# Optimization experiments

Measured on AMD Instinct MI355X. Metric: run time of the kernel, lower is better.

Reference implementation:

```python
import jax, jax.numpy as jnp
import numpy as np

B, T, D, H, C = 64, 512, 128, 512, 256  # batch, seq_len, input_dim, rnn_dim, clf hidden


def _lstm_cell(x, h, c, Wih, Whh, b):
    # PyTorch gate order: i, f, g, o; b = bias_ih + bias_hh
    gates = x @ Wih.T + h @ Whh.T + b  # [B, 4H]
    i, f, g, o = jnp.split(gates, 4, axis=-1)
    c = jax.nn.sigmoid(f) * c + jax.nn.sigmoid(i) * jnp.tanh(g)
    h = jax.nn.sigmoid(o) * jnp.tanh(c)
    return h, c


def _run_lstm2(xs, state, p0, p1):
    # xs: [B, T, in]; state: (h0, c0, h1, c1) each [B, H]
    def step(carry, x_t):
        h0, c0, h1, c1 = carry
        h0, c0 = _lstm_cell(x_t, h0, c0, *p0)
        h1, c1 = _lstm_cell(h0, h1, c1, *p1)
        return (h0, c0, h1, c1), h1
    state, ys = jax.lax.scan(step, state, jnp.swapaxes(xs, 0, 1))
    return jnp.swapaxes(ys, 0, 1), state


def setup_inputs() -> dict:
    key = jax.random.key(0)
    ks = jax.random.split(key, 18)
    s = 0.04  # ~1/sqrt(H), matches torch LSTM init scale
    w = lambda k, shape: (jax.random.normal(k, shape, jnp.float32) * s)
    inp = {
        "x": jax.random.uniform(ks[0], (B, T, D), dtype=jnp.float32),
        "y": (jax.random.uniform(ks[1], (B, T, D), dtype=jnp.float32) > 0.9).astype(jnp.float32),
        "enc_Wih0": w(ks[2], (4 * H, D)), "enc_Whh0": w(ks[3], (4 * H, H)), "enc_b0": w(ks[4], (4 * H,)),
        "enc_Wih1": w(ks[5], (4 * H, H)), "enc_Whh1": w(ks[6], (4 * H, H)), "enc_b1": w(ks[7], (4 * H,)),
        "dec_Wih0": w(ks[8], (4 * H, D)), "dec_Whh0": w(ks[9], (4 * H, H)), "dec_b0": w(ks[10], (4 * H,)),
        "dec_Wih1": w(ks[11], (4 * H, H)), "dec_Whh1": w(ks[12], (4 * H, H)), "dec_b1": w(ks[13], (4 * H,)),
        "clf_W1": w(ks[14], (C, H)), "clf_b1": w(ks[15], (C,)),
        "clf_W2": w(ks[16], (D, C)), "clf_b2": w(ks[17], (D,)),
    }
    return inp


def reference(x, y, enc_Wih0, enc_Whh0, enc_b0, enc_Wih1, enc_Whh1, enc_b1,
              dec_Wih0, dec_Whh0, dec_b0, dec_Wih1, dec_Whh1, dec_b1,
              clf_W1, clf_b1, clf_W2, clf_b2):
    Bc = x.shape[0]
    z = jnp.zeros((Bc, H), x.dtype)
    # encoder: only final (h, c) of both layers is used
    _, state = _run_lstm2(x, (z, z, z, z),
                          (enc_Wih0, enc_Whh0, enc_b0), (enc_Wih1, enc_Whh1, enc_b1))
    # decoder under full teacher forcing: steps t=1..T-1 consume y[:, t-1]
    dec_out, _ = _run_lstm2(y[:, :-1], state,
                            (dec_Wih0, dec_Whh0, dec_b0), (dec_Wih1, dec_Whh1, dec_b1))
    hid = jax.nn.relu(dec_out @ clf_W1.T + clf_b1)          # [B, T-1, C]
    logits = hid @ clf_W2.T + clf_b2                        # [B, T-1, D]
    # outputs[:, 0] stays zero, as in the torch loop starting at t=1
    return jnp.concatenate([jnp.zeros_like(logits[:, :1]), logits], axis=1)
```

## Files before the change

### kernel.cpp

```cpp
#include <hip/hip_runtime.h>
#include <hip/hip_bf16.h>
#include <stdint.h>

#define SMEM_BYTES 150528

using short8  = __attribute__((ext_vector_type(8))) short;
using f32x4   = __attribute__((ext_vector_type(4))) float;
using u32x4   = __attribute__((ext_vector_type(4))) unsigned int;

#define OXBF 0u
#define OYBF 8388608u
#define OWE0 16777216u
#define OWD0 (OWE0 + 2621440u)
#define OWE1 (OWD0 + 2621440u)
#define OWD1 (OWE1 + 4194304u)
#define OWC1 (OWD1 + 4194304u)
#define OWC2 (OWC1 + 262144u)
#define OH0  (OWC2 + 65536u)
#define OH1  (OH0 + 524288u)
#define OHP  (OH1 + 524288u)
#define OFLG (OHP + 262144u)
#define OFC1 (OFLG + 4096u)
#define OFH  (OFLG + 8192u)
#define OFL  (OFLG + 9216u)
#define OH1B (OFLG + 16384u)

static __device__ __forceinline__ unsigned short f2bf(float f){
  union { float f; unsigned u; } v; v.f = f;
  unsigned r = v.u + 0x7FFFu + ((v.u >> 16) & 1u);
  return (unsigned short)(r >> 16);
}
static __device__ __forceinline__ float sigm(float x){ return 1.f/(1.f+__expf(-x)); }
static __device__ __forceinline__ float tanh_(float x){ return 1.f - 2.f/(__expf(2.f*x)+1.f); }

static __device__ __forceinline__ u32x4 ld_cg16(const void* p){
  u32x4 v;
  asm volatile("global_load_dwordx4 %0, %1, off sc0 sc1" : "=v"(v) : "v"(p) : "memory");
  return v;
}
static __device__ __forceinline__ unsigned ld_cg4(const void* p){
  unsigned v;
  asm volatile("global_load_dword %0, %1, off sc0 sc1\n\ts_waitcnt vmcnt(0)"
               : "=v"(v) : "v"(p) : "memory");
  return v;
}
static __device__ __forceinline__ unsigned ld_cg4_async(const void* p){
  unsigned v;
  asm volatile("global_load_dword %0, %1, off sc0 sc1" : "=v"(v) : "v"(p) : "memory");
  return v;
}
static __device__ __forceinline__ void st_cg16(void* p, u32x4 v){
  asm volatile("global_store_dwordx4 %0, %1, off sc0 sc1" :: "v"(p), "v"(v) : "memory");
}
static __device__ __forceinline__ void st_cg4(void* p, unsigned v){
  asm volatile("global_store_dword %0, %1, off sc0 sc1" :: "v"(p), "v"(v) : "memory");
}
static __device__ __forceinline__ void drain_vm(){
  asm volatile("s_waitcnt vmcnt(0)" ::: "memory");
}
static __device__ __forceinline__ bool isS(u32x4 v){
  return (v[0]==0xFFFFFFFFu) | (v[1]==0xFFFFFFFFu) | (v[2]==0xFFFFFFFFu) | (v[3]==0xFFFFFFFFu);
}

__global__ void k_init(float* __restrict__ out, uint8_t* __restrict__ ws){
  int i = blockIdx.x*blockDim.x + threadIdx.x;
  int ns = gridDim.x*blockDim.x;
  uint32_t* r0 = (uint32_t*)(ws + OH0);
  uint32_t* r1 = (uint32_t*)(ws + OH1);
  const int slotw = 65536/4;
  for (int k=i; k<8*slotw; k+=ns){
    unsigned v = (k < 7*slotw) ? 0xFFFFFFFFu : 0u;
    r0[k] = v; r1[k] = v;
  }
  uint32_t* rb = (uint32_t*)(ws + OH1B);
  for (int k=i; k<8*slotw; k+=ns) rb[k] = 0xFFFFFFFFu;
  uint32_t* rp = (uint32_t*)(ws + OHP);
  for (int k=i; k<262144/4; k+=ns) rp[k] = 0xFFFFFFFFu;
  uint32_t* fl = (uint32_t*)(ws + OFLG);
  for (int k=i; k<16384/4; k+=ns) fl[k] = 0u;
  for (int k=i; k<64*128; k+=ns) out[(size_t)(k>>7)*(512*128) + (k&127)] = 0.f;
}

__global__ void k_cvt(const float* __restrict__ x, const float* __restrict__ y,
                      uint8_t* __restrict__ ws){
  unsigned short* xb = (unsigned short*)(ws + OXBF);
  unsigned short* yb = (unsigned short*)(ws + OYBF);
  const int n = 64*512*128;
  int i = blockIdx.x*blockDim.x + threadIdx.x, ns = gridDim.x*blockDim.x;
  for (int k=i; k<n; k+=ns){ xb[k] = f2bf(x[k]); yb[k] = f2bf(y[k]); }
}

__global__ void k_swzgate(const float* __restrict__ Wih, const float* __restrict__ Whh,
                          uint8_t* __restrict__ ws, size_t dstOff, int Kin, int KC, int NKK, int mode){
  unsigned short* dst = (unsigned short*)(ws + dstOff);
  const int total = 2048 * (KC*4);
  int i = blockIdx.x*blockDim.x + threadIdx.x, ns = gridDim.x*blockDim.x;
  for (int idx=i; idx<total; idx+=ns){
    int j = idx & 7;
    int lane = (idx >> 3) & 63;
    int t = idx >> 9;
    int g = t & 3; t >>= 2;
    int kk = t % NKK; t /= NKK;
    int w = t & 3; int ub = t >> 2;
    int off = ((lane>>4)<<3) + j;
    int k = mode ? (kk==0 ? w*32 + off : 128 + w*128 + (kk-1)*32 + off)
                 : (w*KC + kk*32 + off);
    int u = ub*16 + (lane&15);
    int row = g*512 + u;
    float v = (k < Kin) ? Wih[(size_t)row*Kin + k] : Whh[(size_t)row*512 + (k-Kin)];
    dst[idx] = f2bf(v);
  }
}

__global__ void k_swzclf(const float* __restrict__ W, uint8_t* __restrict__ ws,
                         size_t dstOff, int nwgs, int Kw, int Ktot){
  unsigned short* dst = (unsigned short*)(ws + dstOff);
  const int NKK = Kw/32;
  const int total = nwgs*4*NKK*64*8;
  int i = blockIdx.x*blockDim.x + threadIdx.x, ns = gridDim.x*blockDim.x;
  for (int idx=i; idx<total; idx+=ns){
    int j = idx & 7;
    int lane = (idx >> 3) & 63;
    int t = idx >> 9;
    int kk = t % NKK; t /= NKK;
    int w = t & 3; int wg = t >> 2;
    int k = w*Kw + kk*32 + ((lane>>4)<<3) + j;
    int col = wg*16 + (lane&15);
    dst[idx] = f2bf(W[(size_t)col*Ktot + k]);
  }
}

__launch_bounds__(256, 1)
__global__ void k_seq(uint8_t* __restrict__ ws,
                      const float* __restrict__ eb0, const float* __restrict__ eb1,
                      const float* __restrict__ db0, const float* __restrict__ db1,
                      const float* __restrict__ cb1, const float* __restrict__ cb2,
                      float* __restrict__ out){
  __shared__ uint8_t smem[SMEM_BYTES];
  const int wg = blockIdx.x, tid = threadIdx.x;
  const int w = tid>>6, l = tid&63, lr = l&15, lg = l>>4;

  const unsigned short* xb = (const unsigned short*)(ws+OXBF);
  const unsigned short* yb = (const unsigned short*)(ws+OYBF);
  unsigned short* h0r = (unsigned short*)(ws+OH0);
  unsigned short* h1r = (unsigned short*)(ws+OH1);
  unsigned short* h1b = (unsigned short*)(ws+OH1B);
  unsigned short* hpr = (unsigned short*)(ws+OHP);

  short8* BL = (short8*)smem;
  float*  P0 = (float*)(smem + 131072);
  float*  P1 = (float*)(smem + 139776);
  unsigned short* HS = (unsigned short*)(smem + 148480);

  const u32x4 S4 = (u32x4){0xFFFFFFFFu,0xFFFFFFFFu,0xFFFFFFFFu,0xFFFFFFFFu};

  auto loadB = [&](size_t srcOff, int bytes){
    const u32x4* s = (const u32x4*)(ws + srcOff);
    u32x4* d = (u32x4*)smem;
    for (int i = tid; i < bytes/16; i += 256) d[i] = s[i];
  };

  if (wg < 128){
    const bool isC0 = wg < 64;
    const int cwg = isC0 ? wg : wg-64;
    const int bt = cwg>>5, ub = cwg&31;
    const int u = tid&15, ug = ub*16 + u;
    const int bbytes = isC0 ? 81920 : 131072;

    float be[4], bd[4];
    {
      const float* e = isC0 ? eb0 : eb1;
      const float* d = isC0 ? db0 : db1;
      #pragma unroll
      for (int g=0; g<4; ++g){ be[g] = e[g*512+ug]; bd[g] = d[g*512+ug]; }
    }
    loadB((isC0 ? (size_t)OWE0 : (size_t)OWE1) + (size_t)ub*bbytes, bbytes);
    float cS0 = 0.f, cS1 = 0.f;
    __syncthreads();

    for (int t = 0; t < 1023; ++t){
      if (t == 512){
        __syncthreads();
        loadB((isC0 ? (size_t)OWD0 : (size_t)OWD1) + (size_t)ub*bbytes, bbytes);
        __syncthreads();
      }

      const int slotW = t&7, slotR = (t+7)&7, slotC = (t+3)&7;
      unsigned short* pub_base = isC0 ? h0r : ((t >= 512) ? h1b : h1r);

      const bool gateAct = isC0 ? (t >= 4) : (t >= 517);
      const int  ng      = isC0 ? 32 : 16;
      const void* fp = isC0 ? (const void*)(ws + OFC1 + (size_t)(bt*32 + (l&31))*64)
                            : (const void*)(ws + OFH  + (size_t)(l&15)*64);
      unsigned fv = 0u;
      if (w == 0 && l < ng && gateAct) fv = ld_cg4_async(fp);

      f32x4 acc[2][4];
      #pragma unroll
      for (int m=0;m<2;++m)
        #pragma unroll
        for (int g=0;g<4;++g) acc[m][g] = (f32x4){0.f,0.f,0.f,0.f};

      if (isC0){
        const unsigned short* xs = (t<512) ? xb : yb;
        const int tt = (t<512) ? t : t-512;
        short8 ax[2];
        #pragma unroll
        for (int m=0;m<2;++m){
          const int b = bt*32 + m*16 + lr;
          ax[m] = *(const short8*)(xs + ((size_t)b*512 + tt)*128 + w*32 + (lg<<3));
        }
        u32x4 ah[4][2];
        const unsigned short* base = h0r + (size_t)slotR*64*512;
        bool bad;
        do {
          #pragma unroll
          for (int kk=0; kk<4; ++kk)
            #pragma unroll
            for (int m=0;m<2;++m){
              const int b = bt*32 + m*16 + lr;
              ah[kk][m] = ld_cg16(base + (size_t)b*512 + w*128 + kk*32 + (lg<<3));
            }
          drain_vm();
          __builtin_amdgcn_sched_barrier(0);
          bad = false;
          #pragma unroll
          for (int kk=0; kk<4; ++kk)
            #pragma unroll
            for (int m=0;m<2;++m) bad |= isS(ah[kk][m]);
          if (bad) __builtin_amdgcn_s_sleep(1);
        } while (bad);
        __builtin_amdgcn_sched_barrier(0);
        #pragma unroll
        for (int g=0;g<4;++g){
          short8 bf = BL[((w*5+0)*4+g)*64 + l];
          acc[0][g] = __builtin_amdgcn_mfma_f32_16x16x32_bf16(ax[0], bf, acc[0][g],0,0,0);
          acc[1][g] = __builtin_amdgcn_mfma_f32_16x16x32_bf16(ax[1], bf, acc[1][g],0,0,0);
        }
        #pragma unroll
        for (int kk=1; kk<5; ++kk)
          #pragma unroll
          for (int g=0;g<4;++g){
            short8 bf = BL[((w*5+kk)*4+g)*64 + l];
            acc[0][g] = __builtin_amdgcn_mfma_f32_16x16x32_bf16(__builtin_bit_cast(short8, ah[kk-1][0]), bf, acc[0][g],0,0,0);
            acc[1][g] = __builtin_amdgcn_mfma_f32_16x16x32_bf16(__builtin_bit_cast(short8, ah[kk-1][1]), bf, acc[1][g],0,0,0);
          }
      } else {
        u32x4 a[8][2];
        const unsigned short* b0 = h0r + (size_t)slotW*64*512;
        const unsigned short* b1 = ((t-1 >= 512) ? h1b : h1r) + (size_t)slotR*64*512;
        bool bad;
        do {
          #pragma unroll
          for (int kk=0; kk<8; ++kk){
            const int k0 = w*256 + kk*32;
            #pragma unroll
            for (int m=0;m<2;++m){
              const int b = bt*32 + m*16 + lr;
              const void* ap = (k0 < 512)
                ? (const void*)(b0 + (size_t)b*512 + k0 + (lg<<3))
                : (const void*)(b1 + (size_t)b*512 + (k0-512) + (lg<<3));
              a[kk][m] = ld_cg16(ap);
            }
          }
          drain_vm();
          __builtin_amdgcn_sched_barrier(0);
          bad = false;
          #pragma unroll
          for (int kk=0; kk<8; ++kk)
            #pragma unroll
            for (int m=0;m<2;++m) bad |= isS(a[kk][m]);
          if (bad) __builtin_amdgcn_s_sleep(1);
        } while (bad);
        __builtin_amdgcn_sched_barrier(0);
        #pragma unroll
        for (int kk=0; kk<8; ++kk)
          #pragma unroll
          for (int g=0;g<4;++g){
            short8 bf = BL[((w*8+kk)*4+g)*64 + l];
            acc[0][g] = __builtin_amdgcn_mfma_f32_16x16x32_bf16(__builtin_bit_cast(short8, a[kk][0]), bf, acc[0][g],0,0,0);
            acc[1][g] = __builtin_amdgcn_mfma_f32_16x16x32_bf16(__builtin_bit_cast(short8, a[kk][1]), bf, acc[1][g],0,0,0);
          }
      }

      {
        float* P = (w&1) ? P1 : P0;
        if (w < 2){
          #pragma unroll
          for (int m=0;m<2;++m)
            #pragma unroll
            for (int g=0;g<4;++g)
              #pragma unroll
              for (int r=0;r<4;++r)
                P[(m*16 + (lg<<2) + r)*68 + g*16 + lr] = acc[m][g][r];
        }
        __syncthreads();
        if (w >= 2){
          #pragma unroll
          for (int m=0;m<2;++m)
            #pragma unroll
            for (int g=0;g<4;++g)
              #pragma unroll
              for (int r=0;r<4;++r)
                P[(m*16 + (lg<<2) + r)*68 + g*16 + lr] += acc[m][g][r];
        }
        __syncthreads();
      }

      if (w == 0){
        drain_vm();
        __builtin_amdgcn_sched_barrier(0);
        if (gateAct && l < ng){
          const int n0 = isC0 ? (t-4) : (t-516);
          const int need = (n0 < 1) ? 1 : n0;
          int v = (int)fv;
          while (v < need){ v = (int)ld_cg4(fp); __builtin_amdgcn_s_sleep(2); }
        }
        if (t >= 4 && t <= 1019){
          unsigned short* cbase = isC0 ? h0r : ((t+3 >= 512) ? h1b : h1r);
          const int row = l>>1, half = l&1;
          st_cg16(cbase + ((size_t)slotC*64 + bt*32 + row)*512 + ub*16 + half*8, S4);
        }
      }

      const float* bias = (t<512) ? be : bd;
      #pragma unroll
      for (int s=0;s<2;++s){
        const int row = (tid>>4) + s*16;
        const int pi = row*68 + u;
        float gi = P0[pi]      + P1[pi]      + bias[0];
        float gf = P0[pi+16]   + P1[pi+16]   + bias[1];
        float gg = P0[pi+32]   + P1[pi+32]   + bias[2];
        float go = P0[pi+48]   + P1[pi+48]   + bias[3];
        float cprev = s ? cS1 : cS0;
        float c = sigm(gf)*cprev + sigm(gi)*tanh_(gg);
        if (s) cS1 = c; else cS0 = c;
        float h = sigm(go)*tanh_(c);
        HS[row*16 + u] = f2bf(h);
      }
      __syncthreads();
      if (tid < 64){
        u32x4 v = *(const u32x4*)(HS + tid*8);
        const int row = tid>>1, half = tid&1;
        st_cg16(pub_base + ((size_t)slotW*64 + bt*32 + row)*512 + ub*16 + half*8, v);
      }
      if (!isC0 && tid == 0)
        st_cg4(ws + OFC1 + (size_t)(bt*32+ub)*64, (unsigned)(t+1));
    }
  } else if (wg < 144){
    const int hwg = wg - 128;
    const int u = tid&15, col = hwg*16 + u;
    const float bc = cb1[col];
    loadB((size_t)OWC1 + (size_t)hwg*16384, 16384);
    __syncthreads();
    for (int t2 = 0; t2 < 511; ++t2){
      const int slot = t2&7, slotC = (t2+3)&7;
      const bool gateAct = (t2 >= 5);
      const void* fp = (const void*)(ws + OFL + (size_t)(l&7)*64);
      unsigned fv = 0u;
      if (w == 0 && l < 8 && gateAct) fv = ld_cg4_async(fp);

      u32x4 a[4][4];
      const unsigned short* base = h1b + (size_t)slot*64*512;
      bool bad;
      do {
        #pragma unroll
        for (int kk=0; kk<4; ++kk)
          #pragma unroll
          for (int m=0;m<4;++m)
            a[kk][m] = ld_cg16(base + (size_t)(m*16+lr)*512 + w*128 + kk*32 + (lg<<3));
        drain_vm();
        __builtin_amdgcn_sched_barrier(0);
        bad = false;
        #pragma unroll
        for (int kk=0; kk<4; ++kk)
          #pragma unroll
          for (int m=0;m<4;++m) bad |= isS(a[kk][m]);
        if (bad) __builtin_amdgcn_s_sleep(1);
      } while (bad);
      __builtin_amdgcn_sched_barrier(0);
      f32x4 ha[4];
      #pragma unroll
      for (int m=0;m<4;++m) ha[m] = (f32x4){0.f,0.f,0.f,0.f};
      #pragma unroll
      for (int kk=0; kk<4; ++kk){
        short8 bf = BL[(w*4+kk)*64 + l];
        #pragma unroll
        for (int m=0;m<4;++m)
          ha[m] = __builtin_amdgcn_mfma_f32_16x16x32_bf16(__builtin_bit_cast(short8, a[kk][m]), bf, ha[m],0,0,0);
      }
      {
        float* P = (w&1) ? P1 : P0;
        if (w < 2){
          #pragma unroll
          for (int m=0;m<4;++m)
            #pragma unroll
            for (int r=0;r<4;++r)
              P[(m*16 + (lg<<2) + r)*20 + lr] = ha[m][r];
        }
        __syncthreads();
        if (w >= 2){
          #pragma unroll
          for (int m=0;m<4;++m)
            #pragma unroll
            for (int r=0;r<4;++r)
              P[(m*16 + (lg<<2) + r)*20 + lr] += ha[m][r];
        }
        __syncthreads();
      }
      if (w == 0){
        drain_vm();
        __builtin_amdgcn_sched_barrier(0);
        if (gateAct && l < 8){
          const int n0 = t2 - 4;
          const int need = (n0 < 1) ? 1 : n0;
          int v = (int)fv;
          while (v < need){ v = (int)ld_cg4(fp); __builtin_amdgcn_s_sleep(2); }
        }
        if (t2 >= 5 && t2 <= 507){
          #pragma unroll
          for (int q=0;q<2;++q)
            st_cg16(hpr + ((size_t)slotC*64 + l)*256 + hwg*16 + q*8, S4);
        }
      }
      #pragma unroll
      for (int s=0;s<4;++s){
        const int row = (tid>>4) + s*16;
        float v = P0[row*20+u] + P1[row*20+u] + bc;
        HS[row*16 + u] = f2bf(fmaxf(v, 0.f));
      }
      __syncthreads();
      if (tid < 128){
        u32x4 v = *(const u32x4*)(HS + tid*8);
        const int row = tid>>1, half = tid&1;
        st_cg16(hpr + ((size_t)slot*64 + row)*256 + hwg*16 + half*8, v);
      }
      if (tid == 0) st_cg4(ws + OFH + (size_t)hwg*64, (unsigned)(t2+1));
    }
  } else if (wg < 152){
    const int lwg = wg - 144;
    const int u = tid&15, col = lwg*16 + u;
    const float bc = cb2[col];
    loadB((size_t)OWC2 + (size_t)lwg*8192, 8192);
    __syncthreads();
    for (int t3 = 0; t3 < 511; ++t3){
      const int slot = t3&7;
      u32x4 a[2][4];
      const unsigned short* base = hpr + (size_t)slot*64*256;
      bool bad;
      do {
        #pragma unroll
        for (int kk=0; kk<2; ++kk)
          #pragma unroll
          for (int m=0;m<4;++m)
            a[kk][m] = ld_cg16(base + (size_t)(m*16+lr)*256 + w*64 + kk*32 + (lg<<3));
        drain_vm();
        __builtin_amdgcn_sched_barrier(0);
        bad = false;
        #pragma unroll
        for (int kk=0; kk<2; ++kk)
          #pragma unroll
          for (int m=0;m<4;++m) bad |= isS(a[kk][m]);
        if (bad) __builtin_amdgcn_s_sleep(1);
      } while (bad);
      __builtin_amdgcn_sched_barrier(0);
      f32x4 la[4];
      #pragma unroll
      for (int m=0;m<4;++m) la[m] = (f32x4){0.f,0.f,0.f,0.f};
      #pragma unroll
      for (int kk=0; kk<2; ++kk){
        short8 bf = BL[(w*2+kk)*64 + l];
        #pragma unroll
        for (int m=0;m<4;++m)
          la[m] = __builtin_amdgcn_mfma_f32_16x16x32_bf16(__builtin_bit_cast(short8, a[kk][m]), bf, la[m],0,0,0);
      }
      {
        float* P = (w&1) ? P1 : P0;
        if (w < 2){
          #pragma unroll
          for (int m=0;m<4;++m)
            #pragma unroll
            for (int r=0;r<4;++r)
              P[(m*16 + (lg<<2) + r)*20 + lr] = la[m][r];
        }
        __syncthreads();
        if (w >= 2){
          #pragma unroll
          for (int m=0;m<4;++m)
            #pragma unroll
            for (int r=0;r<4;++r)
              P[(m*16 + (lg<<2) + r)*20 + lr] += la[m][r];
        }
        __syncthreads();
      }
      #pragma unroll
      for (int s=0;s<4;++s){
        const int row = (tid>>4) + s*16;
        float v = P0[row*20+u] + P1[row*20+u] + bc;
        out[((size_t)row*512 + (t3+1))*128 + col] = v;
      }
      if (tid == 0) st_cg4(ws + OFL + (size_t)lwg*64, (unsigned)(t3+1));
    }
  }
}

extern "C" void kernel_launch(void* const* d_in, const int* in_sizes, int n_in,
                              void* d_out, int out_size, void* d_ws, size_t ws_size,
                              hipStream_t stream){
  const float* x   = (const float*)d_in[0];
  const float* y   = (const float*)d_in[1];
  const float* eW0 = (const float*)d_in[2];
  const float* eU0 = (const float*)d_in[3];
  const float* eb0 = (const float*)d_in[4];
  const float* eW1 = (const float*)d_in[5];
  const float* eU1 = (const float*)d_in[6];
  const float* eb1 = (const float*)d_in[7];
  const float* dW0 = (const float*)d_in[8];
  const float* dU0 = (const float*)d_in[9];
  const float* db0 = (const float*)d_in[10];
  const float* dW1 = (const float*)d_in[11];
  const float* dU1 = (const float*)d_in[12];
  const float* db1 = (const float*)d_in[13];
  const float* cW1 = (const float*)d_in[14];
  const float* cb1 = (const float*)d_in[15];
  const float* cW2 = (const float*)d_in[16];
  const float* cb2 = (const float*)d_in[17];
  float* out = (float*)d_out;
  uint8_t* ws = (uint8_t*)d_ws;
  (void)in_sizes; (void)n_in; (void)out_size; (void)ws_size;

  k_init<<<dim3(256), dim3(256), 0, stream>>>(out, ws);
  k_cvt<<<dim3(2048), dim3(256), 0, stream>>>(x, y, ws);
  k_swzgate<<<dim3(1280), dim3(256), 0, stream>>>(eW0, eU0, ws, (size_t)OWE0, 128, 160, 5, 1);
  k_swzgate<<<dim3(1280), dim3(256), 0, stream>>>(dW0, dU0, ws, (size_t)OWD0, 128, 160, 5, 1);
  k_swzgate<<<dim3(2048), dim3(256), 0, stream>>>(eW1, eU1, ws, (size_t)OWE1, 512, 256, 8, 0);
  k_swzgate<<<dim3(2048), dim3(256), 0, stream>>>(dW1, dU1, ws, (size_t)OWD1, 512, 256, 8, 0);
  k_swzclf<<<dim3(256), dim3(256), 0, stream>>>(cW1, ws, (size_t)OWC1, 16, 128, 512);
  k_swzclf<<<dim3(64),  dim3(256), 0, stream>>>(cW2, ws, (size_t)OWC2, 8, 64, 256);
  k_seq<<<dim3(152), dim3(256), 0, stream>>>(ws, eb0, eb1, db0, db1, cb1, cb2, out);
}
```

Baseline: 5.779 ms.

## Map pipeline roles to XCDs and use XCD-local cache scope for ring traffic

Launches 256 workgroups and gives each one a role based on wg&7, the XCD it is assumed to land on, so that each group of cooperating workgroups sits on one XCD. A startup probe-and-vote checks that co-residency actually holds. If it does, the h-state rings and flags use sc0-only loads and stores (L2 scope) instead of system-coherent sc0 sc1, which should cut polling latency on the recurrent dependency chain. The layer-0 ring is duplicated into a device-scope copy for cross-XCD readers, and spin loops gain a guard limit. The risks are extra duplicate stores, startup handshake cost, and correctness that depends on the hardware's workgroup-to-XCD mapping.

```diff
diff --git a/kernel.cpp b/kernel.cpp
--- a/kernel.cpp
+++ b/kernel.cpp
@@ -16,14 +16,19 @@
 #define OWD1 (OWE1 + 4194304u)
 #define OWC1 (OWD1 + 4194304u)
 #define OWC2 (OWC1 + 262144u)
-#define OH0  (OWC2 + 65536u)
-#define OH1  (OH0 + 524288u)
-#define OHP  (OH1 + 524288u)
+#define OA0  (OWC2 + 65536u)
+#define OB0  (OA0 + 524288u)
+#define OA1  (OB0 + 524288u)
+#define OB1  (OA1 + 524288u)
+#define OHP  (OB1 + 524288u)
 #define OFLG (OHP + 262144u)
 #define OFC1 (OFLG + 4096u)
 #define OFH  (OFLG + 8192u)
 #define OFL  (OFLG + 9216u)
-#define OH1B (OFLG + 16384u)
+#define OPRB (OFLG + 16384u)
+#define OVOT (OFLG + 32768u)
+
+#define GUARD (1<<19)
 
 static __device__ __forceinline__ unsigned short f2bf(float f){
   union { float f; unsigned u; } v; v.f = f;
@@ -33,27 +38,31 @@
 static __device__ __forceinline__ float sigm(float x){ return 1.f/(1.f+__expf(-x)); }
 static __device__ __forceinline__ float tanh_(float x){ return 1.f - 2.f/(__expf(2.f*x)+1.f); }
 
-static __device__ __forceinline__ u32x4 ld_cg16(const void* p){
+static __device__ __forceinline__ u32x4 ld_r16(const void* p, bool loc){
   u32x4 v;
-  asm volatile("global_load_dwordx4 %0, %1, off sc0 sc1" : "=v"(v) : "v"(p) : "memory");
+  if (loc) asm volatile("global_load_dwordx4 %0, %1, off sc0"     : "=v"(v) : "v"(p) : "memory");
+  else     asm volatile("global_load_dwordx4 %0, %1, off sc0 sc1" : "=v"(v) : "v"(p) : "memory");
   return v;
 }
-static __device__ __forceinline__ unsigned ld_cg4(const void* p){
+static __device__ __forceinline__ void st_r16(void* p, u32x4 v, bool loc){
+  if (loc) asm volatile("global_store_dwordx4 %0, %1, off sc0"     :: "v"(p), "v"(v) : "memory");
+  else     asm volatile("global_store_dwordx4 %0, %1, off sc0 sc1" :: "v"(p), "v"(v) : "memory");
+}
+static __device__ __forceinline__ unsigned ld_f4(const void* p, bool loc){
   unsigned v;
-  asm volatile("global_load_dword %0, %1, off sc0 sc1\n\ts_waitcnt vmcnt(0)"
-               : "=v"(v) : "v"(p) : "memory");
+  if (loc) asm volatile("global_load_dword %0, %1, off sc0\n\ts_waitcnt vmcnt(0)"     : "=v"(v) : "v"(p) : "memory");
+  else     asm volatile("global_load_dword %0, %1, off sc0 sc1\n\ts_waitcnt vmcnt(0)" : "=v"(v) : "v"(p) : "memory");
   return v;
 }
-static __device__ __forceinline__ unsigned ld_cg4_async(const void* p){
+static __device__ __forceinline__ unsigned ld_f4a(const void* p, bool loc){
   unsigned v;
-  asm volatile("global_load_dword %0, %1, off sc0 sc1" : "=v"(v) : "v"(p) : "memory");
+  if (loc) asm volatile("global_load_dword %0, %1, off sc0"     : "=v"(v) : "v"(p) : "memory");
+  else     asm volatile("global_load_dword %0, %1, off sc0 sc1" : "=v"(v) : "v"(p) : "memory");
   return v;
 }
-static __device__ __forceinline__ void st_cg16(void* p, u32x4 v){
-  asm volatile("global_store_dwordx4 %0, %1, off sc0 sc1" :: "v"(p), "v"(v) : "memory");
-}
-static __device__ __forceinline__ void st_cg4(void* p, unsigned v){
-  asm volatile("global_store_dword %0, %1, off sc0 sc1" :: "v"(p), "v"(v) : "memory");
+static __device__ __forceinline__ void st_f4(void* p, unsigned v, bool loc){
+  if (loc) asm volatile("global_store_dword %0, %1, off sc0"     :: "v"(p), "v"(v) : "memory");
+  else     asm volatile("global_store_dword %0, %1, off sc0 sc1" :: "v"(p), "v"(v) : "memory");
 }
 static __device__ __forceinline__ void drain_vm(){
   asm volatile("s_waitcnt vmcnt(0)" ::: "memory");
@@ -65,19 +74,11 @@
 __global__ void k_init(float* __restrict__ out, uint8_t* __restrict__ ws){
   int i = blockIdx.x*blockDim.x + threadIdx.x;
   int ns = gridDim.x*blockDim.x;
-  uint32_t* r0 = (uint32_t*)(ws + OH0);
-  uint32_t* r1 = (uint32_t*)(ws + OH1);
-  const int slotw = 65536/4;
-  for (int k=i; k<8*slotw; k+=ns){
-    unsigned v = (k < 7*slotw) ? 0xFFFFFFFFu : 0u;
-    r0[k] = v; r1[k] = v;
-  }
-  uint32_t* rb = (uint32_t*)(ws + OH1B);
-  for (int k=i; k<8*slotw; k+=ns) rb[k] = 0xFFFFFFFFu;
-  uint32_t* rp = (uint32_t*)(ws + OHP);
-  for (int k=i; k<262144/4; k+=ns) rp[k] = 0xFFFFFFFFu;
+  uint32_t* r = (uint32_t*)(ws + OA0);
+  const int nring = (4*524288 + 262144)/4;
+  for (int k=i; k<nring; k+=ns) r[k] = 0xFFFFFFFFu;
   uint32_t* fl = (uint32_t*)(ws + OFLG);
-  for (int k=i; k<16384/4; k+=ns) fl[k] = 0u;
+  for (int k=i; k<49152/4; k+=ns) fl[k] = 0u;
   for (int k=i; k<64*128; k+=ns) out[(size_t)(k>>7)*(512*128) + (k&127)] = 0.f;
 }
 
@@ -139,12 +140,21 @@
   __shared__ uint8_t smem[SMEM_BYTES];
   const int wg = blockIdx.x, tid = threadIdx.x;
   const int w = tid>>6, l = tid&63, lr = l&15, lg = l>>4;
+  const int xcd = wg & 7, j = wg >> 3;
+
+  int role;
+  if (xcd < 2) role = 0;
+  else if (xcd < 4) role = 1;
+  else if (xcd == 4 && j < 16) role = 2;
+  else if (xcd == 4 && j < 24) role = 3;
+  else return;
 
   const unsigned short* xb = (const unsigned short*)(ws+OXBF);
   const unsigned short* yb = (const unsigned short*)(ws+OYBF);
-  unsigned short* h0r = (unsigned short*)(ws+OH0);
-  unsigned short* h1r = (unsigned short*)(ws+OH1);
-  unsigned short* h1b = (unsigned short*)(ws+OH1B);
+  unsigned short* A0e = (unsigned short*)(ws+OA0);
+  unsigned short* B0e = (unsigned short*)(ws+OB0);
+  unsigned short* A1e = (unsigned short*)(ws+OA1);
+  unsigned short* B1e = (unsigned short*)(ws+OB1);
   unsigned short* hpr = (unsigned short*)(ws+OHP);
 
   short8* BL = (short8*)smem;
@@ -153,6 +163,41 @@
   unsigned short* HS = (unsigned short*)(smem + 148480);
 
   const u32x4 S4 = (u32x4){0xFFFFFFFFu,0xFFFFFFFFu,0xFFFFFFFFu,0xFFFFFFFFu};
+  const u32x4 Z4 = (u32x4){0u,0u,0u,0u};
+
+  bool loc;
+  {
+    const int n   = (role <= 1) ? 32 : 24;
+    const int bas = (role <= 1) ? xcd : 4;
+    if (w == 0){
+      bool ok = true;
+      #pragma unroll 1
+      for (int gen = 1; gen <= 3; ++gen){
+        if (l == 0) st_f4(ws + OPRB + (size_t)wg*64u, (unsigned)gen, true);
+        if (l < n){
+          const void* p = ws + OPRB + (size_t)(bas + 8*l)*64u;
+          int spins = 0; unsigned e;
+          do { e = ld_f4(p, true); } while ((int)e < gen && ++spins < 1024);
+          if ((int)e < gen) ok = false;
+        }
+      }
+      unsigned long long b1 = __ballot(ok);
+      bool wgok = (b1 == ~0ULL);
+      if (l == 0) st_f4(ws + OVOT + (size_t)wg*64u, wgok ? 2u : 1u, false);
+      bool vok = wgok;
+      if (l < n){
+        const void* p = ws + OVOT + (size_t)(bas + 8*l)*64u;
+        unsigned v;
+        do { v = ld_f4(p, false); } while (v == 0u);
+        vok = vok && (v == 2u);
+      }
+      unsigned long long b2 = __ballot(vok);
+      if (l == 0) *(int*)HS = (b2 == ~0ULL) ? 1 : 0;
+    }
+    __syncthreads();
+    loc = (*(volatile int*)HS) != 0;
+    __syncthreads();
+  }
 
   auto loadB = [&](size_t srcOff, int bytes){
     const u32x4* s = (const u32x4*)(ws + srcOff);
@@ -160,12 +205,12 @@
     for (int i = tid; i < bytes/16; i += 256) d[i] = s[i];
   };
 
-  if (wg < 128){
-    const bool isC0 = wg < 64;
-    const int cwg = isC0 ? wg : wg-64;
-    const int bt = cwg>>5, ub = cwg&31;
+  if (role <= 1){
+    const bool isC0 = (role == 0);
+    const int bt = isC0 ? xcd : xcd-2, ub = j;
     const int u = tid&15, ug = ub*16 + u;
     const int bbytes = isC0 ? 81920 : 131072;
+    unsigned short* OWN0 = loc ? A0e : B0e;
 
     float be[4], bd[4];
     {
@@ -186,14 +231,13 @@
       }
 
       const int slotW = t&7, slotR = (t+7)&7, slotC = (t+3)&7;
-      unsigned short* pub_base = isC0 ? h0r : ((t >= 512) ? h1b : h1r);
 
       const bool gateAct = isC0 ? (t >= 4) : (t >= 517);
       const int  ng      = isC0 ? 32 : 16;
       const void* fp = isC0 ? (const void*)(ws + OFC1 + (size_t)(bt*32 + (l&31))*64)
                             : (const void*)(ws + OFH  + (size_t)(l&15)*64);
       unsigned fv = 0u;
-      if (w == 0 && l < ng && gateAct) fv = ld_cg4_async(fp);
+      if (w == 0 && l < ng && gateAct) fv = ld_f4a(fp, false);
 
       f32x4 acc[2][4];
       #pragma unroll
@@ -211,26 +255,33 @@
           ax[m] = *(const short8*)(xs + ((size_t)b*512 + tt)*128 + w*32 + (lg<<3));
         }
         u32x4 ah[4][2];
-        const unsigned short* base = h0r + (size_t)slotR*64*512;
-        bool bad;
-        do {
+        if (t > 0){
+          const unsigned short* base = OWN0 + (size_t)slotR*64*512;
+          int gd = 0; bool bad;
+          do {
+            #pragma unroll
+            for (int kk=0; kk<4; ++kk)
+              #pragma unroll
+              for (int m=0;m<2;++m){
+                const int b = bt*32 + m*16 + lr;
+                ah[kk][m] = ld_r16(base + (size_t)b*512 + w*128 + kk*32 + (lg<<3), loc);
+              }
+            drain_vm();
+            __builtin_amdgcn_sched_barrier(0);
+            bad = false;
+            #pragma unroll
+            for (int kk=0; kk<4; ++kk)
+              #pragma unroll
+              for (int m=0;m<2;++m) bad |= isS(ah[kk][m]);
+            if (bad) __builtin_amdgcn_s_sleep(1);
+          } while (bad && ++gd < GUARD);
+          __builtin_amdgcn_sched_barrier(0);
+        } else {
           #pragma unroll
           for (int kk=0; kk<4; ++kk)
             #pragma unroll
-            for (int m=0;m<2;++m){
-              const int b = bt*32 + m*16 + lr;
-              ah[kk][m] = ld_cg16(base + (size_t)b*512 + w*128 + kk*32 + (lg<<3));
-            }
-          drain_vm();
-          __builtin_amdgcn_sched_barrier(0);
-          bad = false;
-          #pragma unroll
-          for (int kk=0; kk<4; ++kk)
-            #pragma unroll
-            for (int m=0;m<2;++m) bad |= isS(ah[kk][m]);
-          if (bad) __builtin_amdgcn_s_sleep(1);
-        } while (bad);
-        __builtin_amdgcn_sched_barrier(0);
+            for (int m=0;m<2;++m) ah[kk][m] = Z4;
+        }
         #pragma unroll
         for (int g=0;g<4;++g){
           short8 bf = BL[((w*5+0)*4+g)*64 + l];
@@ -247,32 +298,41 @@
           }
       } else {
         u32x4 a[8][2];
-        const unsigned short* b0 = h0r + (size_t)slotW*64*512;
-        const unsigned short* b1 = ((t-1 >= 512) ? h1b : h1r) + (size_t)slotR*64*512;
-        bool bad;
-        do {
-          #pragma unroll
-          for (int kk=0; kk<8; ++kk){
-            const int k0 = w*256 + kk*32;
-            #pragma unroll
-            for (int m=0;m<2;++m){
-              const int b = bt*32 + m*16 + lr;
-              const void* ap = (k0 < 512)
-                ? (const void*)(b0 + (size_t)b*512 + k0 + (lg<<3))
-                : (const void*)(b1 + (size_t)b*512 + (k0-512) + (lg<<3));
-              a[kk][m] = ld_cg16(ap);
-            }
+        const bool wv01 = (w < 2);
+        if (wv01 || t > 0){
+          const unsigned short* base;
+          bool myloc;
+          if (wv01){ base = B0e + (size_t)slotW*64*512; myloc = false; }
+          else {
+            base = (loc ? A1e : (((t-1) >= 512) ? B1e : A1e)) + (size_t)slotR*64*512;
+            myloc = loc;
           }
-          drain_vm();
+          const int kbase = wv01 ? (w*256) : (w*256 - 512);
+          int gd = 0; bool bad;
+          do {
+            #pragma unroll
+            for (int kk=0; kk<8; ++kk)
+              #pragma unroll
+              for (int m=0;m<2;++m){
+                const int b = bt*32 + m*16 + lr;
+                a[kk][m] = ld_r16(base + (size_t)b*512 + kbase + kk*32 + (lg<<3), myloc);
+              }
+            drain_vm();
+            __builtin_amdgcn_sched_barrier(0);
+            bad = false;
+            #pragma unroll
+            for (int kk=0; kk<8; ++kk)
+              #pragma unroll
+              for (int m=0;m<2;++m) bad |= isS(a[kk][m]);
+            if (bad) __builtin_amdgcn_s_sleep(1);
+          } while (bad && ++gd < GUARD);
           __builtin_amdgcn_sched_barrier(0);
-          bad = false;
+        } else {
           #pragma unroll
           for (int kk=0; kk<8; ++kk)
             #pragma unroll
-            for (int m=0;m<2;++m) bad |= isS(a[kk][m]);
-          if (bad) __builtin_amdgcn_s_sleep(1);
-        } while (bad);
-        __builtin_amdgcn_sched_barrier(0);
+            for (int m=0;m<2;++m) a[kk][m] = Z4;
+        }
         #pragma unroll
         for (int kk=0; kk<8; ++kk)
           #pragma unroll
@@ -313,13 +373,23 @@
         if (gateAct && l < ng){
           const int n0 = isC0 ? (t-4) : (t-516);
           const int need = (n0 < 1) ? 1 : n0;
-          int v = (int)fv;
-          while (v < need){ v = (int)ld_cg4(fp); __builtin_amdgcn_s_sleep(2); }
+          int v = (int)fv, gd = 0;
+          while (v < need && ++gd < GUARD){ v = (int)ld_f4(fp, false); __builtin_amdgcn_s_sleep(2); }
         }
         if (t >= 4 && t <= 1019){
-          unsigned short* cbase = isC0 ? h0r : ((t+3 >= 512) ? h1b : h1r);
           const int row = l>>1, half = l&1;
-          st_cg16(cbase + ((size_t)slotC*64 + bt*32 + row)*512 + ub*16 + half*8, S4);
+          const size_t off = ((size_t)slotC*64 + bt*32 + row)*512 + ub*16 + half*8;
+          if (isC0){
+            st_r16(OWN0 + off, S4, loc);
+            if (loc) st_r16(B0e + off, S4, false);
+          } else {
+            if (loc){
+              st_r16(A1e + off, S4, true);
+              if (t+3 >= 512) st_r16(B1e + off, S4, false);
+            } else {
+              st_r16(((t+3 >= 512) ? B1e : A1e) + off, S4, false);
+            }
+          }
         }
       }
 
@@ -342,13 +412,24 @@
       if (tid < 64){
         u32x4 v = *(const u32x4*)(HS + tid*8);
         const int row = tid>>1, half = tid&1;
-        st_cg16(pub_base + ((size_t)slotW*64 + bt*32 + row)*512 + ub*16 + half*8, v);
+        const size_t off = ((size_t)slotW*64 + bt*32 + row)*512 + ub*16 + half*8;
+        if (isC0){
+          st_r16(OWN0 + off, v, loc);
+          if (loc) st_r16(B0e + off, v, false);
+        } else {
+          if (loc){
+            st_r16(A1e + off, v, true);
+            if (t >= 512) st_r16(B1e + off, v, false);
+          } else {
+            st_r16(((t >= 512) ? B1e : A1e) + off, v, false);
+          }
+        }
       }
       if (!isC0 && tid == 0)
-        st_cg4(ws + OFC1 + (size_t)(bt*32+ub)*64, (unsigned)(t+1));
+        st_f4(ws + OFC1 + (size_t)(bt*32+ub)*64, (unsigned)(t+1), false);
     }
-  } else if (wg < 144){
-    const int hwg = wg - 128;
+  } else if (role == 2){
+    const int hwg = j;
     const int u = tid&15, col = hwg*16 + u;
     const float bc = cb1[col];
     loadB((size_t)OWC1 + (size_t)hwg*16384, 16384);
@@ -358,17 +439,17 @@
       const bool gateAct = (t2 >= 5);
       const void* fp = (const void*)(ws + OFL + (size_t)(l&7)*64);
       unsigned fv = 0u;
-      if (w == 0 && l < 8 && gateAct) fv = ld_cg4_async(fp);
+      if (w == 0 && l < 8 && gateAct) fv = ld_f4a(fp, loc);
 
       u32x4 a[4][4];
-      const unsigned short* base = h1b + (size_t)slot*64*512;
-      bool bad;
+      const unsigned short* base = B1e + (size_t)slot*64*512;
+      int gd = 0; bool bad;
       do {
         #pragma unroll
         for (int kk=0; kk<4; ++kk)
           #pragma unroll
           for (int m=0;m<4;++m)
-            a[kk][m] = ld_cg16(base + (size_t)(m*16+lr)*512 + w*128 + kk*32 + (lg<<3));
+            a[kk][m] = ld_r16(base + (size_t)(m*16+lr)*512 + w*128 + kk*32 + (lg<<3), false);
         drain_vm();
         __builtin_amdgcn_sched_barrier(0);
         bad = false;
@@ -377,7 +458,7 @@
           #pragma unroll
           for (int m=0;m<4;++m) bad |= isS(a[kk][m]);
         if (bad) __builtin_amdgcn_s_sleep(1);
-      } while (bad);
+      } while (bad && ++gd < GUARD);
       __builtin_amdgcn_sched_barrier(0);
       f32x4 ha[4];
       #pragma unroll
@@ -414,13 +495,13 @@
         if (gateAct && l < 8){
           const int n0 = t2 - 4;
           const int need = (n0 < 1) ? 1 : n0;
-          int v = (int)fv;
-          while (v < need){ v = (int)ld_cg4(fp); __builtin_amdgcn_s_sleep(2); }
+          int v = (int)fv, g2 = 0;
+          while (v < need && ++g2 < GUARD){ v = (int)ld_f4(fp, loc); __builtin_amdgcn_s_sleep(2); }
         }
         if (t2 >= 5 && t2 <= 507){
           #pragma unroll
           for (int q=0;q<2;++q)
-            st_cg16(hpr + ((size_t)slotC*64 + l)*256 + hwg*16 + q*8, S4);
+            st_r16(hpr + ((size_t)slotC*64 + l)*256 + hwg*16 + q*8, S4, loc);
         }
       }
       #pragma unroll
@@ -433,12 +514,12 @@
       if (tid < 128){
         u32x4 v = *(const u32x4*)(HS + tid*8);
         const int row = tid>>1, half = tid&1;
-        st_cg16(hpr + ((size_t)slot*64 + row)*256 + hwg*16 + half*8, v);
-      }
-      if (tid == 0) st_cg4(ws + OFH + (size_t)hwg*64, (unsigned)(t2+1));
+        st_r16(hpr + ((size_t)slot*64 + row)*256 + hwg*16 + half*8, v, loc);
+      }
+      if (tid == 0) st_f4(ws + OFH + (size_t)hwg*64, (unsigned)(t2+1), false);
     }
-  } else if (wg < 152){
-    const int lwg = wg - 144;
+  } else {
+    const int lwg = j - 16;
     const int u = tid&15, col = lwg*16 + u;
     const float bc = cb2[col];
     loadB((size_t)OWC2 + (size_t)lwg*8192, 8192);
@@ -447,13 +528,13 @@
       const int slot = t3&7;
       u32x4 a[2][4];
       const unsigned short* base = hpr + (size_t)slot*64*256;
-      bool bad;
+      int gd = 0; bool bad;
       do {
         #pragma unroll
         for (int kk=0; kk<2; ++kk)
           #pragma unroll
           for (int m=0;m<4;++m)
-            a[kk][m] = ld_cg16(base + (size_t)(m*16+lr)*256 + w*64 + kk*32 + (lg<<3));
+            a[kk][m] = ld_r16(base + (size_t)(m*16+lr)*256 + w*64 + kk*32 + (lg<<3), loc);
         drain_vm();
         __builtin_amdgcn_sched_barrier(0);
         bad = false;
@@ -462,7 +543,7 @@
           #pragma unroll
           for (int m=0;m<4;++m) bad |= isS(a[kk][m]);
         if (bad) __builtin_amdgcn_s_sleep(1);
-      } while (bad);
+      } while (bad && ++gd < GUARD);
       __builtin_amdgcn_sched_barrier(0);
       f32x4 la[4];
       #pragma unroll
@@ -499,7 +580,7 @@
         float v = P0[row*20+u] + P1[row*20+u] + bc;
         out[((size_t)row*512 + (t3+1))*128 + col] = v;
       }
-      if (tid == 0) st_cg4(ws + OFL + (size_t)lwg*64, (unsigned)(t3+1));
+      if (tid == 0) st_f4(ws + OFL + (size_t)lwg*64, (unsigned)(t3+1), loc);
     }
   }
 }
@@ -537,5 +618,5 @@
   k_swzgate<<<dim3(2048), dim3(256), 0, stream>>>(dW1, dU1, ws, (size_t)OWD1, 512, 256, 8, 0);
   k_swzclf<<<dim3(256), dim3(256), 0, stream>>>(cW1, ws, (size_t)OWC1, 16, 128, 512);
   k_swzclf<<<dim3(64),  dim3(256), 0, stream>>>(cW2, ws, (size_t)OWC2, 8, 64, 256);
-  k_seq<<<dim3(152), dim3(256), 0, stream>>>(ws, eb0, eb1, db0, db1, cb1, cb2, out);
-}
+  k_seq<<<dim3(256), dim3(256), 0, stream>>>(ws, eb0, eb1, db0, db1, cb1, cb2, out);
+}
```

Result: faster. 5.281 ms (-8.6%).
